# Kernel optimization log

Hardware: AMD Instinct MI355X
Metric: run time of the kernel (lower is better)

Reference implementation:

```python
import jax, jax.numpy as jnp
import numpy as np

NUM_ROI = 148
P = 1
Q = 5
N = 131072


def setup_inputs() -> dict:
    key = jax.random.key(0)
    kX, kZ, kWr, kbr, kWf, kbf = jax.random.split(key, 6)
    X = jax.random.normal(kX, (N, P), dtype=jnp.float32)
    Z = jax.random.normal(kZ, (N, Q), dtype=jnp.float32)
    # Stacked per-ROI linear layers (torch nn.Linear default init scale)
    s_r = 1.0 / np.sqrt(Q)
    s_f = 1.0 / np.sqrt(P + Q)
    Wr = jax.random.uniform(kWr, (NUM_ROI, Q), jnp.float32, -s_r, s_r)
    br = jax.random.uniform(kbr, (NUM_ROI,), jnp.float32, -s_r, s_r)
    Wf = jax.random.uniform(kWf, (NUM_ROI, P + Q), jnp.float32, -s_f, s_f)
    bf = jax.random.uniform(kbf, (NUM_ROI,), jnp.float32, -s_f, s_f)
    return {"X": X, "Z": Z, "Wr": Wr, "br": br, "Wf": Wf, "bf": bf}


def reference(X, Z, Wr, br, Wf, bf):
    # combined_XZ: [N, p+q]
    XZ = jnp.concatenate([X, Z], axis=-1)
    # All 148 per-ROI GEMVs batched into two matmuls; output stacked as [roi, N]
    r_out = jnp.einsum("nq,rq->rn", Z, Wr) + br[:, None]   # [148, N]
    f_out = jnp.einsum("nd,rd->rn", XZ, Wf) + bf[:, None]  # [148, N]
    return (r_out, f_out)
```

## Files before the change

### kernel.cpp

```cpp
#include <hip/hip_runtime.h>

#define NUM_ROI 148
#define NQ 5
#define NN 131072
#define ROI_SPLIT 4
#define ROI_PER (NUM_ROI / ROI_SPLIT)

__global__ __launch_bounds__(256) void coconet_kernel(
    const float* __restrict__ X, const float* __restrict__ Z,
    const float* __restrict__ Wr, const float* __restrict__ br,
    const float* __restrict__ Wf, const float* __restrict__ bf,
    float* __restrict__ out)
{
    __shared__ float w[ROI_PER][16];
    const int tid = threadIdx.x;
    const int roiBase = blockIdx.y * ROI_PER;

    if (tid < ROI_PER) {
        const int r = roiBase + tid;
        #pragma unroll
        for (int q = 0; q < NQ; ++q) w[tid][q] = Wr[r * NQ + q];
        w[tid][5] = br[r];
        #pragma unroll
        for (int d = 0; d < 6; ++d) w[tid][6 + d] = Wf[r * 6 + d];
        w[tid][12] = bf[r];
    }
    __syncthreads();

    const int n0 = (blockIdx.x * 256 + tid) * 4;

    const float4 x4 = *reinterpret_cast<const float4*>(X + n0);
    const float x[4] = {x4.x, x4.y, x4.z, x4.w};

    float z[4][NQ];
    {
        const float4* zp = reinterpret_cast<const float4*>(Z + (size_t)n0 * NQ);
        const float4 a = zp[0], b = zp[1], c = zp[2], d = zp[3], e = zp[4];
        const float tmp[20] = {a.x, a.y, a.z, a.w, b.x, b.y, b.z, b.w,
                               c.x, c.y, c.z, c.w, d.x, d.y, d.z, d.w,
                               e.x, e.y, e.z, e.w};
        #pragma unroll
        for (int j = 0; j < 4; ++j)
            #pragma unroll
            for (int q = 0; q < NQ; ++q) z[j][q] = tmp[j * NQ + q];
    }

    float* outR = out + (size_t)roiBase * NN + n0;
    float* outF = out + (size_t)(NUM_ROI + roiBase) * NN + n0;

    for (int i = 0; i < ROI_PER; ++i) {
        const float4 w0 = *reinterpret_cast<const float4*>(&w[i][0]);
        const float4 w1 = *reinterpret_cast<const float4*>(&w[i][4]);
        const float4 w2 = *reinterpret_cast<const float4*>(&w[i][8]);
        const float bfv = w[i][12];
        const float wr[NQ] = {w0.x, w0.y, w0.z, w0.w, w1.x};
        const float brv = w1.y, wfx = w1.z;
        const float wf[NQ] = {w1.w, w2.x, w2.y, w2.z, w2.w};

        float rr[4], ff[4];
        #pragma unroll
        for (int j = 0; j < 4; ++j) {
            float r_ = brv;
            float f_ = fmaf(x[j], wfx, bfv);
            #pragma unroll
            for (int q = 0; q < NQ; ++q) {
                r_ = fmaf(z[j][q], wr[q], r_);
                f_ = fmaf(z[j][q], wf[q], f_);
            }
            rr[j] = r_;
            ff[j] = f_;
        }
        *reinterpret_cast<float4*>(outR) = make_float4(rr[0], rr[1], rr[2], rr[3]);
        *reinterpret_cast<float4*>(outF) = make_float4(ff[0], ff[1], ff[2], ff[3]);
        outR += NN;
        outF += NN;
    }
}

extern "C" void kernel_launch(void* const* d_in, const int* in_sizes, int n_in,
                              void* d_out, int out_size, void* d_ws, size_t ws_size,
                              hipStream_t stream) {
    const float* X  = (const float*)d_in[0];
    const float* Z  = (const float*)d_in[1];
    const float* Wr = (const float*)d_in[2];
    const float* br = (const float*)d_in[3];
    const float* Wf = (const float*)d_in[4];
    const float* bf = (const float*)d_in[5];
    float* out = (float*)d_out;

    dim3 grid(NN / (256 * 4), ROI_SPLIT);
    coconet_kernel<<<grid, 256, 0, stream>>>(X, Z, Wr, br, Wf, bf, out);
}
```

Before: 164.3 us.

## Split ROIs finely across grid, load weights directly, use nontemporal stores

The grid now gives each block 4 ROIs instead of 37, which raises the block count from 512 to 4736 for more parallelism and better tail balance. Weights are read straight from global memory, uniform per block, instead of being staged in shared memory behind a barrier. Output writes become nontemporal vector stores so the large write stream bypasses cache. In exchange, the X and Z inputs are re-read 37 times rather than 4 times, though they are small and likely to hit in cache.

```diff
diff --git a/kernel.cpp b/kernel.cpp
--- a/kernel.cpp
+++ b/kernel.cpp
@@ -3,8 +3,11 @@
 #define NUM_ROI 148
 #define NQ 5
 #define NN 131072
-#define ROI_SPLIT 4
-#define ROI_PER (NUM_ROI / ROI_SPLIT)
+#define ROI_PER 4
+#define NBLK_Y (NUM_ROI / ROI_PER)
+#define NBLK_X (NN / (256 * 4))
+
+typedef float vf4 __attribute__((ext_vector_type(4)));
 
 __global__ __launch_bounds__(256) void coconet_kernel(
     const float* __restrict__ X, const float* __restrict__ Z,
@@ -12,30 +15,17 @@
     const float* __restrict__ Wf, const float* __restrict__ bf,
     float* __restrict__ out)
 {
-    __shared__ float w[ROI_PER][16];
     const int tid = threadIdx.x;
-    const int roiBase = blockIdx.y * ROI_PER;
+    const int n0 = (blockIdx.x * 256 + tid) * 4;
+    const int r0 = blockIdx.y * ROI_PER;
 
-    if (tid < ROI_PER) {
-        const int r = roiBase + tid;
-        #pragma unroll
-        for (int q = 0; q < NQ; ++q) w[tid][q] = Wr[r * NQ + q];
-        w[tid][5] = br[r];
-        #pragma unroll
-        for (int d = 0; d < 6; ++d) w[tid][6 + d] = Wf[r * 6 + d];
-        w[tid][12] = bf[r];
-    }
-    __syncthreads();
-
-    const int n0 = (blockIdx.x * 256 + tid) * 4;
-
-    const float4 x4 = *reinterpret_cast<const float4*>(X + n0);
+    const vf4 x4 = *reinterpret_cast<const vf4*>(X + n0);
     const float x[4] = {x4.x, x4.y, x4.z, x4.w};
 
     float z[4][NQ];
     {
-        const float4* zp = reinterpret_cast<const float4*>(Z + (size_t)n0 * NQ);
-        const float4 a = zp[0], b = zp[1], c = zp[2], d = zp[3], e = zp[4];
+        const vf4* zp = reinterpret_cast<const vf4*>(Z + (size_t)n0 * NQ);
+        const vf4 a = zp[0], b = zp[1], c = zp[2], d = zp[3], e = zp[4];
         const float tmp[20] = {a.x, a.y, a.z, a.w, b.x, b.y, b.z, b.w,
                                c.x, c.y, c.z, c.w, d.x, d.y, d.z, d.w,
                                e.x, e.y, e.z, e.w};
@@ -45,17 +35,20 @@
             for (int q = 0; q < NQ; ++q) z[j][q] = tmp[j * NQ + q];
     }
 
-    float* outR = out + (size_t)roiBase * NN + n0;
-    float* outF = out + (size_t)(NUM_ROI + roiBase) * NN + n0;
+    float* outR = out + (size_t)r0 * NN + n0;
+    float* outF = out + (size_t)(NUM_ROI + r0) * NN + n0;
 
+    #pragma unroll
     for (int i = 0; i < ROI_PER; ++i) {
-        const float4 w0 = *reinterpret_cast<const float4*>(&w[i][0]);
-        const float4 w1 = *reinterpret_cast<const float4*>(&w[i][4]);
-        const float4 w2 = *reinterpret_cast<const float4*>(&w[i][8]);
-        const float bfv = w[i][12];
-        const float wr[NQ] = {w0.x, w0.y, w0.z, w0.w, w1.x};
-        const float brv = w1.y, wfx = w1.z;
-        const float wf[NQ] = {w1.w, w2.x, w2.y, w2.z, w2.w};
+        const int r = r0 + i;
+        float wr[NQ], wf[NQ];
+        #pragma unroll
+        for (int q = 0; q < NQ; ++q) wr[q] = Wr[r * NQ + q];
+        const float brv = br[r];
+        const float wfx = Wf[r * 6 + 0];
+        #pragma unroll
+        for (int q = 0; q < NQ; ++q) wf[q] = Wf[r * 6 + 1 + q];
+        const float bfv = bf[r];
 
         float rr[4], ff[4];
         #pragma unroll
@@ -70,10 +63,10 @@
             rr[j] = r_;
             ff[j] = f_;
         }
-        *reinterpret_cast<float4*>(outR) = make_float4(rr[0], rr[1], rr[2], rr[3]);
-        *reinterpret_cast<float4*>(outF) = make_float4(ff[0], ff[1], ff[2], ff[3]);
-        outR += NN;
-        outF += NN;
+        vf4 rv; rv.x = rr[0]; rv.y = rr[1]; rv.z = rr[2]; rv.w = rr[3];
+        vf4 fv; fv.x = ff[0]; fv.y = ff[1]; fv.z = ff[2]; fv.w = ff[3];
+        __builtin_nontemporal_store(rv, reinterpret_cast<vf4*>(outR + (size_t)i * NN));
+        __builtin_nontemporal_store(fv, reinterpret_cast<vf4*>(outF + (size_t)i * NN));
     }
 }
 
@@ -88,6 +81,6 @@
     const float* bf = (const float*)d_in[5];
     float* out = (float*)d_out;
 
-    dim3 grid(NN / (256 * 4), ROI_SPLIT);
+    dim3 grid(NBLK_X, NBLK_Y);
     coconet_kernel<<<grid, 256, 0, stream>>>(X, Z, Wr, br, Wf, bf, out);
 }
```

Result: slower. 169.0 us (+2.9%).
